# Kernel tuning notes

Measured on AMD Instinct MI355X. Metric: run time of the kernel, lower is better.

Reference implementation:

```python
import jax, jax.numpy as jnp
import numpy as np

NUM_DATA, MAX_SEQ_LEN, NUM_INPUTS = 256, 2048, 256
NUM_HIDDEN, NUM_OUTPUTS = 1024, 256

def _xavier(key, shape):
    fan_in, fan_out = shape
    limit = float(np.sqrt(6.0 / (fan_in + fan_out)))
    return jax.random.uniform(key, shape, jnp.float32, -limit, limit)

def setup_inputs() -> dict:
    key = jax.random.key(0)
    ks = jax.random.split(key, 8)
    return {
        "x": jax.random.normal(ks[0], (NUM_DATA, MAX_SEQ_LEN, NUM_INPUTS), jnp.float32),
        "W_in1": _xavier(ks[1], (NUM_INPUTS, NUM_HIDDEN)),
        "b_in1": jnp.zeros((NUM_HIDDEN,), jnp.float32),
        "W_rec1": _xavier(ks[2], (NUM_HIDDEN, NUM_HIDDEN)),
        "W_in2": _xavier(ks[3], (NUM_INPUTS, NUM_HIDDEN)),
        "b_in2": jnp.zeros((NUM_HIDDEN,), jnp.float32),
        "W_rec2": _xavier(ks[4], (NUM_HIDDEN, NUM_HIDDEN)),
        "W_out": _xavier(ks[5], (NUM_HIDDEN, NUM_OUTPUTS)),
        "b_out": jnp.zeros((NUM_OUTPUTS,), jnp.float32),
    }

def reference(x, W_in1, b_in1, W_rec1, W_in2, b_in2, W_rec2, W_out, b_out):
    num_data, max_seq_len, _ = x.shape
    num_hidden = W_in1.shape[1]

    def step_fn(carry, inp):
        z1, z2 = carry                      # each [max_seq_len, num_hidden]
        x_seq, step = inp                   # x_seq: [max_seq_len, num_inputs]
        z12 = z1 + z2
        z1_new = jnp.tanh(x_seq @ W_in1 + z12 @ W_rec1 + b_in1)
        z2_cand = jnp.tanh(x_seq @ W_in2 + z2 @ W_rec2 + b_in2)
        # Layer2 holds previous state on odd steps
        z2_new = jnp.where((step % 2) == 1, z2, z2_cand)
        z_out = jnp.tanh(z1_new @ W_out + b_out)[-1, :]  # [num_outputs]
        return (z1_new, z2_new), z_out

    z0 = jnp.zeros((max_seq_len, num_hidden), x.dtype)
    steps = jnp.arange(num_data)
    _, out = jax.lax.scan(step_fn, (z0, z0), (x, steps))
    return out  # [num_data, num_outputs]
```

## Files before the change

kernel.cpp:

```cpp
#include <hip/hip_runtime.h>
#include <math.h>

#define ND  256
#define SEQ 2048
#define NI  256
#define NH  1024
#define NO  256

#define RB   64
#define RT   1024
#define HPB  16
#define NHP  (NH + 1)

#define XTB  32
#define OTB  8

#define AL(p)    __hip_atomic_load((p), __ATOMIC_RELAXED, __HIP_MEMORY_SCOPE_AGENT)
#define AS(p,v)  __hip_atomic_store((p), (v), __ATOMIC_RELAXED, __HIP_MEMORY_SCOPE_AGENT)

__global__ void xproj(const float* __restrict__ x,
                      const float* __restrict__ Win1, const float* __restrict__ b1,
                      const float* __restrict__ Win2, const float* __restrict__ b2,
                      float* __restrict__ X1, float* __restrict__ X2) {
    const int   layer = blockIdx.z;
    const int   t0    = blockIdx.y * XTB;
    const int   h     = blockIdx.x * 256 + threadIdx.x;
    const float* W = layer ? Win2 : Win1;
    const float* b = layer ? b2   : b1;
    float*       X = layer ? X2   : X1;

    __shared__ float lx[XTB][NI];
    for (int idx = threadIdx.x; idx < XTB * NI; idx += 256) {
        int r = idx >> 8, c = idx & (NI - 1);
        lx[r][c] = x[(size_t)(t0 + r) * SEQ * NI + (size_t)(SEQ - 1) * NI + c];
    }
    __syncthreads();

    float acc[XTB];
    float bias = b[h];
    #pragma unroll
    for (int r = 0; r < XTB; ++r) acc[r] = bias;

    for (int i = 0; i < NI; ++i) {
        float wv = W[i * NH + h];
        #pragma unroll
        for (int r = 0; r < XTB; ++r) acc[r] += lx[r][i] * wv;
    }
    #pragma unroll
    for (int r = 0; r < XTB; ++r) X[(t0 + r) * NH + h] = acc[r];
}

__launch_bounds__(RT, 1)
__global__ void recur(const float* __restrict__ Wr1, const float* __restrict__ Wr2,
                      const float* __restrict__ X1,  const float* __restrict__ X2,
                      float* Z12, float* Z2, float* Z1hist, int* bar) {
    __shared__ float lW1[HPB][NHP];
    __shared__ float lW2[HPB][NHP];
    __shared__ float sz [NH];
    __shared__ float sz2[NH];

    const int tid = threadIdx.x;
    const int h0  = blockIdx.x * HPB;

    for (int idx = tid; idx < HPB * NH; idx += RT) {
        int hw = idx & (HPB - 1);
        int k  = idx >> 4;
        lW1[hw][k] = Wr1[(size_t)k * NH + h0 + hw];
        lW2[hw][k] = Wr2[(size_t)k * NH + h0 + hw];
    }
    __syncthreads();

    const int w = tid >> 6;
    const int l = tid & 63;
    const int h = h0 + w;

    float z2h = 0.0f;
    int   cur = 0;

    int* cnt = bar + 32;
    int* gen = bar + 64;

    for (int t = 0; t < ND; ++t) {
        const bool even = (t & 1) == 0;

        sz[tid] = AL(Z12 + cur * NH + tid);
        if (even) sz2[tid] = AL(Z2 + ((t >> 1) & 1) * NH + tid);
        __syncthreads();

        float xv1 = X1[t * NH + h];
        float r1 = 0.0f, r2 = 0.0f, xv2 = 0.0f;
        #pragma unroll
        for (int j = 0; j < 16; ++j) {
            int k = l + 64 * j;
            r1 += sz[k] * lW1[w][k];
        }
        if (even) {
            xv2 = X2[t * NH + h];
            #pragma unroll
            for (int j = 0; j < 16; ++j) {
                int k = l + 64 * j;
                r2 += sz2[k] * lW2[w][k];
            }
        }
        #pragma unroll
        for (int off = 32; off; off >>= 1) {
            r1 += __shfl_xor(r1, off, 64);
            r2 += __shfl_xor(r2, off, 64);
        }

        if (l == 0) {
            float z1n = tanhf(xv1 + r1);
            if (even) z2h = tanhf(xv2 + r2);
            Z1hist[t * NH + h] = z1n;
            AS(Z12 + (cur ^ 1) * NH + h, z1n + z2h);
            if (even) AS(Z2 + (((t >> 1) & 1) ^ 1) * NH + h, z2h);
        }
        cur ^= 1;

        if (t == ND - 1) break;

        __builtin_amdgcn_s_waitcnt(0);
        __syncthreads();
        if (tid == 0) {
            int g = AL(gen);
            int a = __hip_atomic_fetch_add(cnt, 1, __ATOMIC_RELAXED,
                                           __HIP_MEMORY_SCOPE_AGENT);
            if (a == RB - 1) {
                AS(cnt, 0);
                AS(gen, g + 1);
            } else {
                while (AL(gen) == g) { }
            }
        }
        __syncthreads();
    }
}

__global__ void outproj(const float* __restrict__ Z1hist,
                        const float* __restrict__ Wout,
                        const float* __restrict__ bout,
                        float* __restrict__ out) {
    const int t0 = blockIdx.x * OTB;
    const int o  = threadIdx.x;

    __shared__ float lz[OTB][NH];
    for (int idx = threadIdx.x; idx < OTB * NH; idx += 256) {
        int r = idx >> 10, c = idx & (NH - 1);
        lz[r][c] = Z1hist[(t0 + r) * NH + c];
    }
    __syncthreads();

    float acc[OTB];
    float bias = bout[o];
    #pragma unroll
    for (int r = 0; r < OTB; ++r) acc[r] = bias;

    for (int hh = 0; hh < NH; ++hh) {
        float wv = Wout[hh * NO + o];
        #pragma unroll
        for (int r = 0; r < OTB; ++r) acc[r] += lz[r][hh] * wv;
    }
    #pragma unroll
    for (int r = 0; r < OTB; ++r) out[(t0 + r) * NO + o] = tanhf(acc[r]);
}

extern "C" void kernel_launch(void* const* d_in, const int* in_sizes, int n_in,
                              void* d_out, int out_size, void* d_ws, size_t ws_size,
                              hipStream_t stream) {
    const float* x     = (const float*)d_in[0];
    const float* Win1  = (const float*)d_in[1];
    const float* b1    = (const float*)d_in[2];
    const float* Wr1   = (const float*)d_in[3];
    const float* Win2  = (const float*)d_in[4];
    const float* b2    = (const float*)d_in[5];
    const float* Wr2   = (const float*)d_in[6];
    const float* Wout  = (const float*)d_in[7];
    const float* bout  = (const float*)d_in[8];
    float* out = (float*)d_out;

    float* ws   = (float*)d_ws;
    float* Z12  = ws;
    float* Z2   = Z12 + 2 * NH;
    int*   bar  = (int*)(Z2 + 2 * NH);
    float* Z1h  = (float*)(bar + 128);
    float* X1   = Z1h + ND * NH;
    float* X2   = X1 + ND * NH;

    hipMemsetAsync(Z12, 0, (4 * NH) * sizeof(float) + 128 * sizeof(int), stream);

    dim3 xg(NH / 256, ND / XTB, 2);
    xproj<<<xg, 256, 0, stream>>>(x, Win1, b1, Win2, b2, X1, X2);

    recur<<<RB, RT, 0, stream>>>(Wr1, Wr2, X1, X2, Z12, Z2, Z1h, bar);

    outproj<<<ND / OTB, NO, 0, stream>>>(Z1h, Wout, bout, out);
}
```

Measured before the change: 1.696 ms.

## Replace grid barrier with tag-bit flagged state words and vectorize dot products

Removes the global atomic counter barrier between time steps. Each hidden-state word instead carries a 2-bit step tag in its low mantissa bits, and consumers spin until every word they need has the expected tag. The per-step dot products now read LDS with float4 loads over a padded row layout, and the X loads are hoisted above the wait. This trades a little precision (2 mantissa bits) and per-element polling traffic for shorter per-step synchronization latency.

Result: slower. 1.750 ms (+3.2%).

```diff
diff --git a/kernel.cpp b/kernel.cpp
--- a/kernel.cpp
+++ b/kernel.cpp
@@ -10,7 +10,7 @@
 #define RB   64
 #define RT   1024
 #define HPB  16
-#define NHP  (NH + 1)
+#define NHP  1028
 
 #define XTB  32
 #define OTB  8
@@ -53,10 +53,10 @@
 __launch_bounds__(RT, 1)
 __global__ void recur(const float* __restrict__ Wr1, const float* __restrict__ Wr2,
                       const float* __restrict__ X1,  const float* __restrict__ X2,
-                      float* Z12, float* Z2, float* Z1hist, int* bar) {
+                      unsigned* ZB, unsigned* Z2B, float* Z1hist) {
     __shared__ float lW1[HPB][NHP];
     __shared__ float lW2[HPB][NHP];
-    __shared__ float sz [NH];
+    __shared__ float sz [2][NH];
     __shared__ float sz2[NH];
 
     const int tid = threadIdx.x;
@@ -75,64 +75,71 @@
     const int h = h0 + w;
 
     float z2h = 0.0f;
-    int   cur = 0;
-
-    int* cnt = bar + 32;
-    int* gen = bar + 64;
 
     for (int t = 0; t < ND; ++t) {
         const bool even = (t & 1) == 0;
 
-        sz[tid] = AL(Z12 + cur * NH + tid);
-        if (even) sz2[tid] = AL(Z2 + ((t >> 1) & 1) * NH + tid);
+        float xv1 = X1[t * NH + h];
+        float xv2 = even ? X2[t * NH + h] : 0.0f;
+
+        unsigned tg1 = (unsigned)t & 3u;
+        unsigned* p1 = ZB + (t & 1) * NH + tid;
+        unsigned wv;
+        if (even) {
+            unsigned tg2 = (unsigned)(t >> 1) & 3u;
+            unsigned* p2 = Z2B + ((t >> 1) & 1) * NH + tid;
+            unsigned yv;
+            do { wv = AL(p1); yv = AL(p2); }
+            while ((((wv ^ tg1) & 3u) | ((yv ^ tg2) & 3u)) != 0u);
+            sz2[tid] = __uint_as_float(yv);
+        } else {
+            do { wv = AL(p1); } while ((wv & 3u) != tg1);
+        }
+        sz[t & 1][tid] = __uint_as_float(wv);
         __syncthreads();
 
-        float xv1 = X1[t * NH + h];
-        float r1 = 0.0f, r2 = 0.0f, xv2 = 0.0f;
+        const float4* zv  = (const float4*)sz[t & 1];
+        const float4* wv1 = (const float4*)(&lW1[w][0]);
+        float r1 = 0.0f, r2 = 0.0f;
         #pragma unroll
-        for (int j = 0; j < 16; ++j) {
-            int k = l + 64 * j;
-            r1 += sz[k] * lW1[w][k];
+        for (int jj = 0; jj < 4; ++jj) {
+            float4 a = zv[4 * l + jj], bq = wv1[4 * l + jj];
+            r1 += a.x * bq.x + a.y * bq.y + a.z * bq.z + a.w * bq.w;
         }
         if (even) {
-            xv2 = X2[t * NH + h];
+            const float4* z2v = (const float4*)sz2;
+            const float4* wv2 = (const float4*)(&lW2[w][0]);
             #pragma unroll
-            for (int j = 0; j < 16; ++j) {
-                int k = l + 64 * j;
-                r2 += sz2[k] * lW2[w][k];
+            for (int jj = 0; jj < 4; ++jj) {
+                float4 a = z2v[4 * l + jj], bq = wv2[4 * l + jj];
+                r2 += a.x * bq.x + a.y * bq.y + a.z * bq.z + a.w * bq.w;
             }
-        }
-        #pragma unroll
-        for (int off = 32; off; off >>= 1) {
-            r1 += __shfl_xor(r1, off, 64);
-            r2 += __shfl_xor(r2, off, 64);
+            #pragma unroll
+            for (int off = 32; off; off >>= 1) {
+                r1 += __shfl_xor(r1, off, 64);
+                r2 += __shfl_xor(r2, off, 64);
+            }
+        } else {
+            #pragma unroll
+            for (int off = 32; off; off >>= 1)
+                r1 += __shfl_xor(r1, off, 64);
         }
 
         if (l == 0) {
             float z1n = tanhf(xv1 + r1);
             if (even) z2h = tanhf(xv2 + r2);
             Z1hist[t * NH + h] = z1n;
-            AS(Z12 + (cur ^ 1) * NH + h, z1n + z2h);
-            if (even) AS(Z2 + (((t >> 1) & 1) ^ 1) * NH + h, z2h);
-        }
-        cur ^= 1;
-
-        if (t == ND - 1) break;
-
-        __builtin_amdgcn_s_waitcnt(0);
-        __syncthreads();
-        if (tid == 0) {
-            int g = AL(gen);
-            int a = __hip_atomic_fetch_add(cnt, 1, __ATOMIC_RELAXED,
-                                           __HIP_MEMORY_SCOPE_AGENT);
-            if (a == RB - 1) {
-                AS(cnt, 0);
-                AS(gen, g + 1);
-            } else {
-                while (AL(gen) == g) { }
+            if (t < ND - 1) {
+                unsigned zi = (__float_as_uint(z1n + z2h) & ~3u)
+                            | ((unsigned)(t + 1) & 3u);
+                AS(ZB + ((t + 1) & 1) * NH + h, zi);
+                if (even) {
+                    unsigned yi = (__float_as_uint(z2h) & ~3u)
+                                | ((unsigned)((t >> 1) + 1) & 3u);
+                    AS(Z2B + (((t >> 1) & 1) ^ 1) * NH + h, yi);
+                }
             }
         }
-        __syncthreads();
     }
 }
 
@@ -178,20 +185,19 @@
     const float* bout  = (const float*)d_in[8];
     float* out = (float*)d_out;
 
-    float* ws   = (float*)d_ws;
-    float* Z12  = ws;
-    float* Z2   = Z12 + 2 * NH;
-    int*   bar  = (int*)(Z2 + 2 * NH);
-    float* Z1h  = (float*)(bar + 128);
-    float* X1   = Z1h + ND * NH;
-    float* X2   = X1 + ND * NH;
-
-    hipMemsetAsync(Z12, 0, (4 * NH) * sizeof(float) + 128 * sizeof(int), stream);
+    unsigned* ws  = (unsigned*)d_ws;
+    unsigned* ZB  = ws;
+    unsigned* Z2B = ZB + 2 * NH;
+    float*    Z1h = (float*)(Z2B + 2 * NH);
+    float*    X1  = Z1h + ND * NH;
+    float*    X2  = X1 + ND * NH;
+
+    hipMemsetAsync(ZB, 0, 4 * NH * sizeof(unsigned), stream);
 
     dim3 xg(NH / 256, ND / XTB, 2);
     xproj<<<xg, 256, 0, stream>>>(x, Win1, b1, Win2, b2, X1, X2);
 
-    recur<<<RB, RT, 0, stream>>>(Wr1, Wr2, X1, X2, Z12, Z2, Z1h, bar);
+    recur<<<RB, RT, 0, stream>>>(Wr1, Wr2, X1, X2, ZB, Z2B, Z1h);
 
     outproj<<<ND / OTB, NO, 0, stream>>>(Z1h, Wout, bout, out);
 }
```
